# Kernel optimization log

Hardware: AMD Instinct MI355X
Metric: run time of the kernel (lower is better)

Reference implementation:

```python
import jax, jax.numpy as jnp
import numpy as np

B, T, S, D, H = 8, 512, 512, 512, 8
DH = D // H
EPS = 1e-5


def _ln(x, g, b):
    m = x.mean(-1, keepdims=True)
    v = x.var(-1, keepdims=True)
    return (x - m) / jnp.sqrt(v + EPS) * g + b


def setup_inputs() -> dict:
    key = jax.random.key(0)
    ks = jax.random.split(key, 24)
    w = lambda k, shp: (jax.random.normal(k, shp, jnp.float32) * 0.02)
    causal = jnp.where(jnp.tril(jnp.ones((T, T), bool)), 0.0, -1e9).astype(jnp.float32)
    return {
        "tgt": jax.random.normal(ks[0], (B, T, D), jnp.float32),
        "memory": jax.random.normal(ks[1], (B, S, D), jnp.float32),
        "tgt_mask": causal,
        "gate": jax.random.uniform(ks[2], (T, D), jnp.float32),
        # self-attn params (torch MultiheadAttention packed in_proj layout)
        "sa_in_w": w(ks[3], (3 * D, D)), "sa_in_b": w(ks[4], (3 * D,)),
        "sa_out_w": w(ks[5], (D, D)), "sa_out_b": w(ks[6], (D,)),
        # cross-attn params
        "ca_in_w": w(ks[7], (3 * D, D)), "ca_in_b": w(ks[8], (3 * D,)),
        "ca_out_w": w(ks[9], (D, D)), "ca_out_b": w(ks[10], (D,)),
        # FFN
        "ff1_w": w(ks[11], (4 * D, D)), "ff1_b": w(ks[12], (4 * D,)),
        "ff2_w": w(ks[13], (D, 4 * D)), "ff2_b": w(ks[14], (D,)),
        # layernorms
        "ln1_g": jnp.ones((D,), jnp.float32), "ln1_b": jnp.zeros((D,), jnp.float32),
        "ln2_g": jnp.ones((D,), jnp.float32), "ln2_b": jnp.zeros((D,), jnp.float32),
        "ln3_g": jnp.ones((D,), jnp.float32), "ln3_b": jnp.zeros((D,), jnp.float32),
    }


def reference(tgt, memory, tgt_mask, gate,
              sa_in_w, sa_in_b, sa_out_w, sa_out_b,
              ca_in_w, ca_in_b, ca_out_w, ca_out_b,
              ff1_w, ff1_b, ff2_w, ff2_b,
              ln1_g, ln1_b, ln2_g, ln2_b, ln3_g, ln3_b):
    b, t, d = tgt.shape
    s = memory.shape[1]
    scale = 1.0 / jnp.sqrt(jnp.float32(DH))

    # ---- self attention (standard batched MHA, additive mask) ----
    wq, wk, wv = jnp.split(sa_in_w, 3, axis=0)
    bq, bk, bv = jnp.split(sa_in_b, 3, axis=0)
    q = ((tgt @ wq.T + bq).reshape(b, t, H, DH)) * scale
    k = (tgt @ wk.T + bk).reshape(b, t, H, DH)
    v = (tgt @ wv.T + bv).reshape(b, t, H, DH)
    scores = jnp.einsum('bthd,bshd->bhts', q, k) + tgt_mask  # (B,H,T,T)
    attn = jax.nn.softmax(scores, axis=-1)
    sa = jnp.einsum('bhts,bshd->bthd', attn, v).reshape(b, t, d) @ sa_out_w.T + sa_out_b
    x = _ln(tgt + sa, ln1_g, ln1_b)

    # ---- gated cross attention ----
    # Original: key_{b,t,s} = W_k(gate_t * memory_{b,s}) + b_k materialized as (B*T,S,D).
    # Faithful refactor: distribute W_k, fold (q W_k) with gate into the query side.
    cwq, cwk, cwv = jnp.split(ca_in_w, 3, axis=0)
    cbq, cbk, cbv = jnp.split(ca_in_b, 3, axis=0)
    cq = ((x @ cwq.T + cbq).reshape(b, t, H, DH)) * scale          # (B,T,H,dh)
    wk_h = cwk.reshape(H, DH, d)                                    # (H,dh,D)
    qW = jnp.einsum('bthe,hed->bthd', cq, wk_h)                     # (B,T,H,D)
    cscores = jnp.einsum('bthd,td,bsd->bhts', qW, gate, memory)     # (B,H,T,S)
    bk_h = cbk.reshape(H, DH)
    cscores = cscores + jnp.einsum('bthe,he->bht', cq, bk_h)[..., None]
    cattn = jax.nn.softmax(cscores, axis=-1)
    cv = (memory @ cwv.T + cbv).reshape(b, s, H, DH)
    ca = jnp.einsum('bhts,bshe->bthe', cattn, cv).reshape(b, t, d) @ ca_out_w.T + ca_out_b
    x = _ln(x + ca, ln2_g, ln2_b)

    # ---- FFN ----
    ff = jax.nn.relu(x @ ff1_w.T + ff1_b) @ ff2_w.T + ff2_b
    return _ln(x + ff, ln3_g, ln3_b)
```

## Files before the change

kernel.cpp:

```cpp
#include <hip/hip_runtime.h>
#include <hip/hip_bf16.h>

#define BB 8
#define TT 512
#define SS 512
#define DD 512
#define HH 8

typedef __attribute__((ext_vector_type(8))) short bf16x8;
typedef __attribute__((ext_vector_type(4))) float f32x4;
typedef unsigned short u16;

__device__ __forceinline__ u16 f2b(float f) {
    __hip_bfloat16 h = __float2bfloat16(f);
    return *reinterpret_cast<u16*>(&h);
}
__device__ __forceinline__ float b2f(u16 v) {
    unsigned int u = ((unsigned int)v) << 16;
    return __builtin_bit_cast(float, u);
}
__device__ __forceinline__ void g2lds16(const void* g, void* l) {
    __builtin_amdgcn_global_load_lds(
        (const __attribute__((address_space(1))) void*)g,
        (__attribute__((address_space(3))) void*)l, 16, 0, 0);
}
template <int N> __device__ __forceinline__ void waitvm();
template <> __device__ __forceinline__ void waitvm<0>()  { asm volatile("s_waitcnt vmcnt(0)" ::: "memory"); }
template <> __device__ __forceinline__ void waitvm<4>()  { asm volatile("s_waitcnt vmcnt(4)" ::: "memory"); }
template <> __device__ __forceinline__ void waitvm<6>()  { asm volatile("s_waitcnt vmcnt(6)" ::: "memory"); }
template <> __device__ __forceinline__ void waitvm<8>()  { asm volatile("s_waitcnt vmcnt(8)" ::: "memory"); }
template <> __device__ __forceinline__ void waitvm<18>() { asm volatile("s_waitcnt vmcnt(18)" ::: "memory"); }
__device__ __forceinline__ void barrier_raw() {
    asm volatile("" ::: "memory");
    __builtin_amdgcn_s_barrier();
    asm volatile("" ::: "memory");
}

struct CastSegs {
    const float* s[9];
    u16* d[9];
    int cum[10];
};
__global__ __launch_bounds__(256) void cast_multi(CastSegs sg) {
    const int total = sg.cum[9];
    for (int i = blockIdx.x * 256 + threadIdx.x; i < total; i += gridDim.x * 256) {
        int k = 0;
#pragma unroll
        for (int j = 1; j < 9; ++j) k += (i >= sg.cum[j]);
        const int loc = i - sg.cum[k];
        float4 v = ((const float4*)sg.s[k])[loc];
        ushort4 u;
        u.x = f2b(v.x); u.y = f2b(v.y); u.z = f2b(v.z); u.w = f2b(v.w);
        ((ushort4*)sg.d[k])[loc] = u;
    }
}

__global__ __launch_bounds__(256) void wkt_kernel(const float* __restrict__ w,
                                                  u16* __restrict__ o) {
    const int idx = blockIdx.x * 256 + threadIdx.x;
    const int h = idx >> 15, d = (idx >> 6) & 511, e = idx & 63;
    o[idx] = f2b(w[(size_t)(512 + h * 64 + e) * 512 + d]);
}

template <int TM, int TN, bool RELU, bool GATE>
__global__ __launch_bounds__(256) void gemm_bf16(
    const u16* __restrict__ A, int lda, long az,
    const u16* __restrict__ Bw, int ldb, long bz,
    const float* __restrict__ bias, const float* __restrict__ biasB,
    const float* __restrict__ gate,
    u16* __restrict__ C, int ldo, long cz,
    int K, float alpha, float alphaB) {
    __shared__ __align__(16) u16 As[2][TM * 64];
    __shared__ __align__(16) u16 Bs[2][TN * 64];
    const int tid = threadIdx.x;
    const int wave = tid >> 6, lane = tid & 63;
    const int lm = lane & 15, lg = lane >> 4;
    const int wm = wave >> 1, wn = wave & 1;
    const int m0 = blockIdx.y * TM, n0 = blockIdx.x * TN;
    A += (size_t)blockIdx.z * az;
    Bw += (size_t)blockIdx.z * bz;
    C += (size_t)blockIdx.z * cz;
    constexpr int MI = TM / 32;
    constexpr int FN = TN / 32;
    constexpr int LPS = MI + FN;

    f32x4 acc[MI][FN];
#pragma unroll
    for (int mi = 0; mi < MI; ++mi)
#pragma unroll
        for (int ni = 0; ni < FN; ++ni) acc[mi][ni] = (f32x4){0.f, 0.f, 0.f, 0.f};

    const int srow = lane >> 3;
    const int sbyte = ((lane & 7) << 4) ^ (srow << 4);
    const int xk = (lm & 7) << 4;

    auto stage = [&](int buf, int kt) {
#pragma unroll
        for (int j = 0; j < MI; ++j) {
            const int r = wave * (TM / 4) + j * 8;
            g2lds16((const char*)(A + (size_t)(m0 + r + srow) * lda + kt) + sbyte,
                    (char*)As[buf] + (size_t)r * 128);
        }
#pragma unroll
        for (int j = 0; j < FN; ++j) {
            const int r = wave * (TN / 4) + j * 8;
            g2lds16((const char*)(Bw + (size_t)(n0 + r + srow) * ldb + kt) + sbyte,
                    (char*)Bs[buf] + (size_t)r * 128);
        }
    };

    stage(0, 0);
    const int NK = K >> 6;
    for (int t = 0; t < NK; ++t) {
        const int cur = t & 1;
        if (t + 1 < NK) { stage(cur ^ 1, (t + 1) << 6); waitvm<LPS>(); }
        else            { waitvm<0>(); }
        barrier_raw();
#pragma unroll
        for (int kh = 0; kh < 2; ++kh) {
            const int cb = kh * 64 + lg * 16;
            bf16x8 af[MI], bfr[FN];
#pragma unroll
            for (int mi = 0; mi < MI; ++mi) {
                const int row = wm * (TM / 2) + mi * 16 + lm;
                af[mi] = *(const bf16x8*)((const char*)As[cur] + row * 128 + (cb ^ xk));
            }
#pragma unroll
            for (int ni = 0; ni < FN; ++ni) {
                const int row = wn * (TN / 2) + ni * 16 + lm;
                bfr[ni] = *(const bf16x8*)((const char*)Bs[cur] + row * 128 + (cb ^ xk));
            }
#pragma unroll
            for (int mi = 0; mi < MI; ++mi)
#pragma unroll
                for (int ni = 0; ni < FN; ++ni)
                    acc[mi][ni] = __builtin_amdgcn_mfma_f32_16x16x32_bf16(
                        af[mi], bfr[ni], acc[mi][ni], 0, 0, 0);
        }
        barrier_raw();
    }

    const float* bp = blockIdx.z ? biasB : bias;
    const float al = blockIdx.z ? alphaB : alpha;
#pragma unroll
    for (int mi = 0; mi < MI; ++mi)
#pragma unroll
        for (int ni = 0; ni < FN; ++ni)
#pragma unroll
            for (int r = 0; r < 4; ++r) {
                const int m = m0 + wm * (TM / 2) + mi * 16 + lg * 4 + r;
                const int n = n0 + wn * (TN / 2) + ni * 16 + lm;
                float v = acc[mi][ni][r];
                if constexpr (GATE) v *= gate[(size_t)(m & 511) * 512 + n];
                else                v = (v + bp[n]) * al;
                if constexpr (RELU) v = fmaxf(v, 0.f);
                C[(size_t)m * ldo + n] = f2b(v);
            }
}

__global__ __launch_bounds__(256) void flash_self(const u16* __restrict__ QKV,
                                                  u16* __restrict__ out) {
    const int t0 = blockIdx.x * 64, h = blockIdx.y, b = blockIdx.z;
    const int tid = threadIdx.x, wave = tid >> 6, lane = tid & 63;
    const int lm = lane & 15, lg = lane >> 4;
    __shared__ __align__(16) u16 Ks[32 * 64];
    __shared__ __align__(16) u16 Vt[64][40];
    __shared__ __align__(16) u16 P[4][16][40];

    const int tw = t0 + wave * 16;
    const size_t qrow = (size_t)(b * TT + tw + lm) * 1536 + h * 64;
    bf16x8 qf[2];
    qf[0] = *(const bf16x8*)(QKV + qrow + lg * 8);
    qf[1] = *(const bf16x8*)(QKV + qrow + 32 + lg * 8);

    float m_run[4], l_run[4];
    f32x4 oacc[4];
#pragma unroll
    for (int r = 0; r < 4; ++r) { m_run[r] = -3e38f; l_run[r] = 0.f; }
#pragma unroll
    for (int nt = 0; nt < 4; ++nt) oacc[nt] = (f32x4){0.f, 0.f, 0.f, 0.f};

    const int srow = lane >> 3, sbyte = ((lane & 7) << 4) ^ (srow << 4);
    const int xk = (lm & 7) << 4;
    const int smax = t0 + 64;
    for (int s0 = 0; s0 < smax; s0 += 32) {
        if (s0) __syncthreads();
        g2lds16((const char*)(QKV + (size_t)(b * TT + s0 + wave * 8 + srow) * 1536 +
                              512 + h * 64) + sbyte,
                (char*)Ks + wave * 1024);
        {
            const int s = tid & 31, d0 = (tid >> 5) * 8;
            bf16x8 vv = *(const bf16x8*)(QKV + (size_t)(b * TT + s0 + s) * 1536 +
                                         1024 + h * 64 + d0);
#pragma unroll
            for (int j = 0; j < 8; ++j) Vt[d0 + j][s] = (u16)vv[j];
        }
        __syncthreads();
        if (s0 <= tw + 15) {
            f32x4 sc0 = (f32x4){0.f, 0.f, 0.f, 0.f};
            f32x4 sc1 = (f32x4){0.f, 0.f, 0.f, 0.f};
#pragma unroll
            for (int f = 0; f < 2; ++f) {
                const int cb = f * 64 + lg * 16;
                bf16x8 k0 = *(const bf16x8*)((const char*)Ks + lm * 128 + (cb ^ xk));
                bf16x8 k1 = *(const bf16x8*)((const char*)Ks + (16 + lm) * 128 + (cb ^ xk));
                sc0 = __builtin_amdgcn_mfma_f32_16x16x32_bf16(qf[f], k0, sc0, 0, 0, 0);
                sc1 = __builtin_amdgcn_mfma_f32_16x16x32_bf16(qf[f], k1, sc1, 0, 0, 0);
            }
            float sv0[4], sv1[4], tm[4];
#pragma unroll
            for (int r = 0; r < 4; ++r) {
                const int t = tw + lg * 4 + r;
                sv0[r] = sc0[r] * 0.125f + ((s0 + lm) <= t ? 0.f : -1e9f);
                sv1[r] = sc1[r] * 0.125f + ((s0 + 16 + lm) <= t ? 0.f : -1e9f);
                tm[r] = fmaxf(sv0[r], sv1[r]);
            }
#pragma unroll
            for (int off = 1; off < 16; off <<= 1)
#pragma unroll
                for (int r = 0; r < 4; ++r) tm[r] = fmaxf(tm[r], __shfl_xor(tm[r], off));
            float fac[4], rs[4];
#pragma unroll
            for (int r = 0; r < 4; ++r) {
                const float mn = fmaxf(m_run[r], tm[r]);
                fac[r] = __expf(m_run[r] - mn);
                m_run[r] = mn;
                const float p0 = __expf(sv0[r] - mn);
                const float p1 = __expf(sv1[r] - mn);
                P[wave][lg * 4 + r][lm] = f2b(p0);
                P[wave][lg * 4 + r][16 + lm] = f2b(p1);
                rs[r] = p0 + p1;
            }
#pragma unroll
            for (int off = 1; off < 16; off <<= 1)
#pragma unroll
                for (int r = 0; r < 4; ++r) rs[r] += __shfl_xor(rs[r], off);
#pragma unroll
            for (int r = 0; r < 4; ++r) l_run[r] = l_run[r] * fac[r] + rs[r];
#pragma unroll
            for (int nt = 0; nt < 4; ++nt)
#pragma unroll
                for (int r = 0; r < 4; ++r) oacc[nt][r] *= fac[r];
            const bf16x8 pf = *(const bf16x8*)&P[wave][lm][lg * 8];
#pragma unroll
            for (int nt = 0; nt < 4; ++nt) {
                const bf16x8 vf = *(const bf16x8*)&Vt[nt * 16 + lm][lg * 8];
                oacc[nt] = __builtin_amdgcn_mfma_f32_16x16x32_bf16(pf, vf, oacc[nt], 0, 0, 0);
            }
        }
    }
#pragma unroll
    for (int nt = 0; nt < 4; ++nt)
#pragma unroll
        for (int r = 0; r < 4; ++r)
            out[(size_t)(b * TT + tw + lg * 4 + r) * DD + h * 64 + nt * 16 + lm] =
                f2b(oacc[nt][r] / l_run[r]);
}

__global__ __launch_bounds__(128, 2) void flash_cross(
    const u16* __restrict__ QW, const u16* __restrict__ Kmem,
    const u16* __restrict__ CV, u16* __restrict__ out) {
    const int t0 = blockIdx.x * 64, h = blockIdx.y, b = blockIdx.z;
    const int tid = threadIdx.x, wave = tid >> 6, lane = tid & 63;
    const int lm = lane & 15, lg = lane >> 4;
    __shared__ __align__(16) u16 Ks[2][32 * 512];
    __shared__ __align__(16) u16 Vt[2][64][40];
    __shared__ __align__(16) u16 P[2][32][40];

    const int tq = t0 + wave * 32;
    const size_t qrowA = (size_t)(b * TT + tq + lm) * 4096 + h * 512;
    const size_t qrowB = qrowA + (size_t)16 * 4096;
    bf16x8 qfA[16], qfB[16];
#pragma unroll
    for (int f = 0; f < 16; ++f) {
        qfA[f] = *(const bf16x8*)(QW + qrowA + f * 32 + lg * 8);
        qfB[f] = *(const bf16x8*)(QW + qrowB + f * 32 + lg * 8);
    }

    float mA[4], lA[4], mB[4], lB[4];
    f32x4 oA[4], oB[4];
#pragma unroll
    for (int r = 0; r < 4; ++r) { mA[r] = -3e38f; lA[r] = 0.f; mB[r] = -3e38f; lB[r] = 0.f; }
#pragma unroll
    for (int nt = 0; nt < 4; ++nt) { oA[nt] = (f32x4){0.f,0.f,0.f,0.f}; oB[nt] = (f32x4){0.f,0.f,0.f,0.f}; }

    const int xk = (lm & 7) << 4;
    const int sV = tid & 31, dV = (tid >> 5) * 16;

    auto stageK = [&](int buf, int s0) {
#pragma unroll
        for (int j = 0; j < 16; ++j) {
            const int row = wave * 16 + j;
            g2lds16((const char*)(Kmem + ((size_t)b * SS + s0 + row) * 512) +
                        ((lane * 16) ^ ((j & 7) << 4)),
                    (char*)Ks[buf] + row * 1024);
        }
    };
    auto vload0 = [&](int s0) -> bf16x8 {
        return *(const bf16x8*)(CV + ((size_t)b * SS + s0 + sV) * 512 + h * 64 + dV);
    };
    auto vload1 = [&](int s0) -> bf16x8 {
        return *(const bf16x8*)(CV + ((size_t)b * SS + s0 + sV) * 512 + h * 64 + dV + 8);
    };

    stageK(0, 0);
    bf16x8 vr0 = vload0(0), vr1 = vload1(0), vn0, vn1;
    for (int c = 0; c < 16; ++c) {
        const int cur = c & 1;
        if (c + 1 < 16) {
            stageK(cur ^ 1, (c + 1) * 32);
            vn0 = vload0((c + 1) * 32);
            vn1 = vload1((c + 1) * 32);
            waitvm<18>();
        } else {
            waitvm<0>();
        }
#pragma unroll
        for (int j = 0; j < 8; ++j) {
            Vt[cur][dV + j][sV] = (u16)vr0[j];
            Vt[cur][dV + 8 + j][sV] = (u16)vr1[j];
        }
        asm volatile("s_waitcnt lgkmcnt(0)" ::: "memory");
        barrier_raw();
        f32x4 sA0 = (f32x4){0.f,0.f,0.f,0.f}, sA1 = (f32x4){0.f,0.f,0.f,0.f};
        f32x4 sB0 = (f32x4){0.f,0.f,0.f,0.f}, sB1 = (f32x4){0.f,0.f,0.f,0.f};
#pragma unroll
        for (int f = 0; f < 16; ++f) {
            const int cb = f * 64 + lg * 16;
            bf16x8 k0 = *(const bf16x8*)((const char*)Ks[cur] + lm * 1024 + (cb ^ xk));
            bf16x8 k1 = *(const bf16x8*)((const char*)Ks[cur] + (16 + lm) * 1024 + (cb ^ xk));
            sA0 = __builtin_amdgcn_mfma_f32_16x16x32_bf16(qfA[f], k0, sA0, 0, 0, 0);
            sA1 = __builtin_amdgcn_mfma_f32_16x16x32_bf16(qfA[f], k1, sA1, 0, 0, 0);
            sB0 = __builtin_amdgcn_mfma_f32_16x16x32_bf16(qfB[f], k0, sB0, 0, 0, 0);
            sB1 = __builtin_amdgcn_mfma_f32_16x16x32_bf16(qfB[f], k1, sB1, 0, 0, 0);
        }
        float tmA[4], tmB[4];
#pragma unroll
        for (int r = 0; r < 4; ++r) {
            tmA[r] = fmaxf(sA0[r], sA1[r]);
            tmB[r] = fmaxf(sB0[r], sB1[r]);
        }
#pragma unroll
        for (int off = 1; off < 16; off <<= 1)
#pragma unroll
            for (int r = 0; r < 4; ++r) {
                tmA[r] = fmaxf(tmA[r], __shfl_xor(tmA[r], off));
                tmB[r] = fmaxf(tmB[r], __shfl_xor(tmB[r], off));
            }
        float facA[4], facB[4], rsA[4], rsB[4];
#pragma unroll
        for (int r = 0; r < 4; ++r) {
            const float mnA = fmaxf(mA[r], tmA[r]);
            facA[r] = __expf(mA[r] - mnA); mA[r] = mnA;
            const float pA0 = __expf(sA0[r] - mnA);
            const float pA1 = __expf(sA1[r] - mnA);
            P[wave][lg * 4 + r][lm] = f2b(pA0);
            P[wave][lg * 4 + r][16 + lm] = f2b(pA1);
            rsA[r] = pA0 + pA1;
            const float mnB = fmaxf(mB[r], tmB[r]);
            facB[r] = __expf(mB[r] - mnB); mB[r] = mnB;
            const float pB0 = __expf(sB0[r] - mnB);
            const float pB1 = __expf(sB1[r] - mnB);
            P[wave][16 + lg * 4 + r][lm] = f2b(pB0);
            P[wave][16 + lg * 4 + r][16 + lm] = f2b(pB1);
            rsB[r] = pB0 + pB1;
        }
#pragma unroll
        for (int off = 1; off < 16; off <<= 1)
#pragma unroll
            for (int r = 0; r < 4; ++r) {
                rsA[r] += __shfl_xor(rsA[r], off);
                rsB[r] += __shfl_xor(rsB[r], off);
            }
#pragma unroll
        for (int r = 0; r < 4; ++r) {
            lA[r] = lA[r] * facA[r] + rsA[r];
            lB[r] = lB[r] * facB[r] + rsB[r];
        }
#pragma unroll
        for (int nt = 0; nt < 4; ++nt)
#pragma unroll
            for (int r = 0; r < 4; ++r) { oA[nt][r] *= facA[r]; oB[nt][r] *= facB[r]; }
        const bf16x8 pfA = *(const bf16x8*)&P[wave][lm][lg * 8];
        const bf16x8 pfB = *(const bf16x8*)&P[wave][16 + lm][lg * 8];
#pragma unroll
        for (int nt = 0; nt < 4; ++nt) {
            const bf16x8 vf = *(const bf16x8*)&Vt[cur][nt * 16 + lm][lg * 8];
            oA[nt] = __builtin_amdgcn_mfma_f32_16x16x32_bf16(pfA, vf, oA[nt], 0, 0, 0);
            oB[nt] = __builtin_amdgcn_mfma_f32_16x16x32_bf16(pfB, vf, oB[nt], 0, 0, 0);
        }
        barrier_raw();
        vr0 = vn0; vr1 = vn1;
    }
#pragma unroll
    for (int nt = 0; nt < 4; ++nt)
#pragma unroll
        for (int r = 0; r < 4; ++r) {
            out[(size_t)(b * TT + tq + lg * 4 + r) * DD + h * 64 + nt * 16 + lm] =
                f2b(oA[nt][r] / lA[r]);
            out[(size_t)(b * TT + tq + 16 + lg * 4 + r) * DD + h * 64 + nt * 16 + lm] =
                f2b(oB[nt][r] / lB[r]);
        }
}

template <bool R1B>
__global__ __launch_bounds__(256) void add_ln(
    const void* __restrict__ R1v, const u16* __restrict__ R2,
    const float* __restrict__ g, const float* __restrict__ bta,
    float* __restrict__ outf, u16* __restrict__ outb) {
    const int row = blockIdx.x, tid = threadIdx.x;
    float x0, x1;
    if constexpr (R1B) {
        ushort2 a = ((const ushort2*)((const u16*)R1v + (size_t)row * DD))[tid];
        x0 = b2f(a.x); x1 = b2f(a.y);
    } else {
        float2 a = ((const float2*)((const float*)R1v + (size_t)row * DD))[tid];
        x0 = a.x; x1 = a.y;
    }
    ushort2 c = ((const ushort2*)(R2 + (size_t)row * DD))[tid];
    x0 += b2f(c.x); x1 += b2f(c.y);

    __shared__ float2 red[256];
    red[tid] = make_float2(x0 + x1, x0 * x0 + x1 * x1);
    __syncthreads();
#pragma unroll
    for (int o = 128; o > 0; o >>= 1) {
        if (tid < o) {
            red[tid].x += red[tid + o].x;
            red[tid].y += red[tid + o].y;
        }
        __syncthreads();
    }
    const float mean = red[0].x * (1.f / 512.f);
    const float var = red[0].y * (1.f / 512.f) - mean * mean;
    const float rstd = rsqrtf(var + 1e-5f);
    const int i = tid * 2;
    const float y0 = (x0 - mean) * rstd * g[i] + bta[i];
    const float y1 = (x1 - mean) * rstd * g[i + 1] + bta[i + 1];
    if (outf) ((float2*)(outf + (size_t)row * DD))[tid] = make_float2(y0, y1);
    if (outb) {
        ushort2 ub; ub.x = f2b(y0); ub.y = f2b(y1);
        ((ushort2*)(outb + (size_t)row * DD))[tid] = ub;
    }
}

extern "C" void kernel_launch(void* const* d_in, const int* in_sizes, int n_in,
                              void* d_out, int out_size, void* d_ws, size_t ws_size,
                              hipStream_t stream) {
    const float* tgt      = (const float*)d_in[0];
    const float* memory   = (const float*)d_in[1];
    const float* gate     = (const float*)d_in[3];
    const float* sa_in_w  = (const float*)d_in[4];
    const float* sa_in_b  = (const float*)d_in[5];
    const float* sa_out_w = (const float*)d_in[6];
    const float* sa_out_b = (const float*)d_in[7];
    const float* ca_in_w  = (const float*)d_in[8];
    const float* ca_in_b  = (const float*)d_in[9];
    const float* ca_out_w = (const float*)d_in[10];
    const float* ca_out_b = (const float*)d_in[11];
    const float* ff1_w    = (const float*)d_in[12];
    const float* ff1_b    = (const float*)d_in[13];
    const float* ff2_w    = (const float*)d_in[14];
    const float* ff2_b    = (const float*)d_in[15];
    const float* ln1_g    = (const float*)d_in[16];
    const float* ln1_b    = (const float*)d_in[17];
    const float* ln2_g    = (const float*)d_in[18];
    const float* ln2_b    = (const float*)d_in[19];
    const float* ln3_g    = (const float*)d_in[20];
    const float* ln3_b    = (const float*)d_in[21];

    u16* ws16     = (u16*)d_ws;
    u16* QKVb     = ws16;
    u16* sa_preb  = ws16 + 6291456;
    u16* PRJb     = ws16 + 8388608;
    u16* X1b      = ws16 + 10485760;
    u16* memb     = ws16 + 12582912;
    u16* CQb      = ws16 + 14680064;
    u16* CVb      = ws16 + 16777216;
    u16* QW       = ws16 + 18874368;
    u16* ca_preb  = ws16 + 35651584;
    u16* PRJ2b    = ws16 + 37748736;
    u16* X2b      = ws16 + 39845888;
    u16* HHb      = ws16 + 41943040;
    u16* F1b      = ws16 + 50331648;
    u16* Wreg     = ws16 + 52428800;
    u16* sa_in_wb = Wreg;
    u16* sa_out_wb= Wreg + 786432;
    u16* ca_wq_b  = Wreg + 1048576;
    u16* ca_wv_b  = Wreg + 1310720;
    u16* WkT      = Wreg + 1572864;
    u16* ca_out_wb= Wreg + 1835008;
    u16* ff1_wb   = Wreg + 2097152;
    u16* ff2_wb   = Wreg + 3145728;
    u16* tgtb     = ws16 + 56623104;
    float* outf   = (float*)d_out;

    const dim3 blk(256);

    CastSegs sg;
    sg.s[0]=tgt; sg.s[1]=memory; sg.s[2]=sa_in_w; sg.s[3]=sa_out_w;
    sg.s[4]=ca_in_w; sg.s[5]=ca_in_w + (size_t)1024*512; sg.s[6]=ca_out_w;
    sg.s[7]=ff1_w; sg.s[8]=ff2_w;
    sg.d[0]=tgtb; sg.d[1]=memb; sg.d[2]=sa_in_wb; sg.d[3]=sa_out_wb;
    sg.d[4]=ca_wq_b; sg.d[5]=ca_wv_b; sg.d[6]=ca_out_wb;
    sg.d[7]=ff1_wb; sg.d[8]=ff2_wb;
    {
        const int n4[9] = {524288,524288,196608,65536,65536,65536,65536,262144,262144};
        int c = 0;
        for (int i = 0; i < 9; ++i) { sg.cum[i] = c; c += n4[i]; }
        sg.cum[9] = c;
    }
    cast_multi<<<2048, blk, 0, stream>>>(sg);
    wkt_kernel<<<1024, blk, 0, stream>>>(ca_in_w, WkT);

    gemm_bf16<128,128,false,false><<<dim3(12,32,1), blk, 0, stream>>>(
        tgtb,512,0, sa_in_wb,512,0, sa_in_b,sa_in_b,nullptr,
        QKVb,1536,0, 512, 1.f,1.f);
    flash_self<<<dim3(8,8,8), blk, 0, stream>>>(QKVb, sa_preb);
    gemm_bf16<64,64,false,false><<<dim3(8,64,1), blk, 0, stream>>>(
        sa_preb,512,0, sa_out_wb,512,0, sa_out_b,sa_out_b,nullptr,
        PRJb,512,0, 512, 1.f,1.f);
    add_ln<false><<<4096, blk, 0, stream>>>(tgt, PRJb, ln1_g, ln1_b, nullptr, X1b);
    gemm_bf16<64,64,false,false><<<dim3(8,64,2), blk, 0, stream>>>(
        X1b,512,2097152, ca_wq_b,512,262144, ca_in_b, ca_in_b+1024, nullptr,
        CQb,512,2097152, 512, 0.125f, 1.f);
    gemm_bf16<64,64,false,true><<<dim3(8,64,8), blk, 0, stream>>>(
        CQb,512,64, WkT,64,32768, nullptr,nullptr,gate,
        QW,4096,512, 64, 1.f,1.f);
    flash_cross<<<dim3(8,8,8), dim3(128), 0, stream>>>(QW, memb, CVb, ca_preb);
    gemm_bf16<64,64,false,false><<<dim3(8,64,1), blk, 0, stream>>>(
        ca_preb,512,0, ca_out_wb,512,0, ca_out_b,ca_out_b,nullptr,
        PRJ2b,512,0, 512, 1.f,1.f);
    add_ln<true><<<4096, blk, 0, stream>>>(X1b, PRJ2b, ln2_g, ln2_b, nullptr, X2b);
    gemm_bf16<128,128,true,false><<<dim3(16,32,1), blk, 0, stream>>>(
        X2b,512,0, ff1_wb,512,0, ff1_b,ff1_b,nullptr,
        HHb,2048,0, 512, 1.f,1.f);
    gemm_bf16<64,64,false,false><<<dim3(8,64,1), blk, 0, stream>>>(
        HHb,2048,0, ff2_wb,2048,0, ff2_b,ff2_b,nullptr,
        F1b,512,0, 2048, 1.f,1.f);
    add_ln<true><<<4096, blk, 0, stream>>>(X2b, F1b, ln3_g, ln3_b, outf, nullptr);

    (void)in_sizes; (void)n_in; (void)out_size; (void)ws_size;
}
```

Baseline: 219.6 us.

## Single-buffer K tile in flash_cross and overlap its load with softmax

Cuts the cross-attention K staging buffer in LDS from double to single buffering, roughly halving per-block shared memory so more blocks can be resident per CU. It also drops the min-blocks launch bound. The prefetch of the next K and V chunk is moved to just after the QK MFMAs and a barrier, so it overlaps with the softmax and PV work instead of the whole previous iteration. The cost is less overlap time before the wait at the end of each iteration, which could expose load latency, plus an extra barrier per chunk.

```diff
diff --git a/kernel.cpp b/kernel.cpp
--- a/kernel.cpp
+++ b/kernel.cpp
@@ -29,7 +29,7 @@
 template <> __device__ __forceinline__ void waitvm<4>()  { asm volatile("s_waitcnt vmcnt(4)" ::: "memory"); }
 template <> __device__ __forceinline__ void waitvm<6>()  { asm volatile("s_waitcnt vmcnt(6)" ::: "memory"); }
 template <> __device__ __forceinline__ void waitvm<8>()  { asm volatile("s_waitcnt vmcnt(8)" ::: "memory"); }
-template <> __device__ __forceinline__ void waitvm<18>() { asm volatile("s_waitcnt vmcnt(18)" ::: "memory"); }
+template <> __device__ __forceinline__ void waitvm<16>() { asm volatile("s_waitcnt vmcnt(16)" ::: "memory"); }
 __device__ __forceinline__ void barrier_raw() {
     asm volatile("" ::: "memory");
     __builtin_amdgcn_s_barrier();
@@ -257,13 +257,13 @@
                 f2b(oacc[nt][r] / l_run[r]);
 }
 
-__global__ __launch_bounds__(128, 2) void flash_cross(
+__global__ __launch_bounds__(128) void flash_cross(
     const u16* __restrict__ QW, const u16* __restrict__ Kmem,
     const u16* __restrict__ CV, u16* __restrict__ out) {
     const int t0 = blockIdx.x * 64, h = blockIdx.y, b = blockIdx.z;
     const int tid = threadIdx.x, wave = tid >> 6, lane = tid & 63;
     const int lm = lane & 15, lg = lane >> 4;
-    __shared__ __align__(16) u16 Ks[2][32 * 512];
+    __shared__ __align__(16) u16 Ks[32 * 512];
     __shared__ __align__(16) u16 Vt[2][64][40];
     __shared__ __align__(16) u16 P[2][32][40];
 
@@ -287,13 +287,13 @@
     const int xk = (lm & 7) << 4;
     const int sV = tid & 31, dV = (tid >> 5) * 16;
 
-    auto stageK = [&](int buf, int s0) {
+    auto stageK = [&](int s0) {
 #pragma unroll
         for (int j = 0; j < 16; ++j) {
             const int row = wave * 16 + j;
             g2lds16((const char*)(Kmem + ((size_t)b * SS + s0 + row) * 512) +
                         ((lane * 16) ^ ((j & 7) << 4)),
-                    (char*)Ks[buf] + row * 1024);
+                    (char*)Ks + row * 1024);
         }
     };
     auto vload0 = [&](int s0) -> bf16x8 {
@@ -303,36 +303,36 @@
         return *(const bf16x8*)(CV + ((size_t)b * SS + s0 + sV) * 512 + h * 64 + dV + 8);
     };
 
-    stageK(0, 0);
-    bf16x8 vr0 = vload0(0), vr1 = vload1(0), vn0, vn1;
+    bf16x8 vr0 = vload0(0), vr1 = vload1(0);
+    stageK(0);
+    waitvm<0>();
+#pragma unroll
+    for (int j = 0; j < 8; ++j) {
+        Vt[0][dV + j][sV] = (u16)vr0[j];
+        Vt[0][dV + 8 + j][sV] = (u16)vr1[j];
+    }
+    asm volatile("s_waitcnt lgkmcnt(0)" ::: "memory");
+    barrier_raw();
+
     for (int c = 0; c < 16; ++c) {
         const int cur = c & 1;
-        if (c + 1 < 16) {
-            stageK(cur ^ 1, (c + 1) * 32);
-            vn0 = vload0((c + 1) * 32);
-            vn1 = vload1((c + 1) * 32);
-            waitvm<18>();
-        } else {
-            waitvm<0>();
-        }
-#pragma unroll
-        for (int j = 0; j < 8; ++j) {
-            Vt[cur][dV + j][sV] = (u16)vr0[j];
-            Vt[cur][dV + 8 + j][sV] = (u16)vr1[j];
-        }
-        asm volatile("s_waitcnt lgkmcnt(0)" ::: "memory");
-        barrier_raw();
         f32x4 sA0 = (f32x4){0.f,0.f,0.f,0.f}, sA1 = (f32x4){0.f,0.f,0.f,0.f};
         f32x4 sB0 = (f32x4){0.f,0.f,0.f,0.f}, sB1 = (f32x4){0.f,0.f,0.f,0.f};
 #pragma unroll
         for (int f = 0; f < 16; ++f) {
             const int cb = f * 64 + lg * 16;
-            bf16x8 k0 = *(const bf16x8*)((const char*)Ks[cur] + lm * 1024 + (cb ^ xk));
-            bf16x8 k1 = *(const bf16x8*)((const char*)Ks[cur] + (16 + lm) * 1024 + (cb ^ xk));
+            bf16x8 k0 = *(const bf16x8*)((const char*)Ks + lm * 1024 + (cb ^ xk));
+            bf16x8 k1 = *(const bf16x8*)((const char*)Ks + (16 + lm) * 1024 + (cb ^ xk));
             sA0 = __builtin_amdgcn_mfma_f32_16x16x32_bf16(qfA[f], k0, sA0, 0, 0, 0);
             sA1 = __builtin_amdgcn_mfma_f32_16x16x32_bf16(qfA[f], k1, sA1, 0, 0, 0);
             sB0 = __builtin_amdgcn_mfma_f32_16x16x32_bf16(qfB[f], k0, sB0, 0, 0, 0);
             sB1 = __builtin_amdgcn_mfma_f32_16x16x32_bf16(qfB[f], k1, sB1, 0, 0, 0);
+        }
+        barrier_raw();
+        if (c < 15) {
+            vr0 = vload0((c + 1) * 32);
+            vr1 = vload1((c + 1) * 32);
+            stageK((c + 1) * 32);
         }
         float tmA[4], tmB[4];
 #pragma unroll
@@ -389,8 +389,17 @@
             oA[nt] = __builtin_amdgcn_mfma_f32_16x16x32_bf16(pfA, vf, oA[nt], 0, 0, 0);
             oB[nt] = __builtin_amdgcn_mfma_f32_16x16x32_bf16(pfB, vf, oB[nt], 0, 0, 0);
         }
-        barrier_raw();
-        vr0 = vn0; vr1 = vn1;
+        if (c < 15) {
+            waitvm<16>();
+#pragma unroll
+            for (int j = 0; j < 8; ++j) {
+                Vt[cur ^ 1][dV + j][sV] = (u16)vr0[j];
+                Vt[cur ^ 1][dV + 8 + j][sV] = (u16)vr1[j];
+            }
+            waitvm<0>();
+            asm volatile("s_waitcnt lgkmcnt(0)" ::: "memory");
+            barrier_raw();
+        }
     }
 #pragma unroll
     for (int nt = 0; nt < 4; ++nt)
```

Measured after the change: 227.1 us. 3.4% more time.

## Split fused cross-attention into scores GEMM plus separate softmax-PV kernel

Applied to the files above, without the earlier changes.

Replaces the fused flash-style cross attention (K-dim 512 per head, low occupancy, 128-thread blocks) with two kernels. A tiled 128x128 GEMM writes full fp32 score matrices to workspace, then a second kernel does a single-pass softmax and the P·V MFMA with V held transposed in LDS. This trades the online-softmax bookkeeping and poor tile reuse for a large round trip of fp32 scores through global memory (64 MB written and read) and one extra launch.

```diff
diff --git a/kernel.cpp b/kernel.cpp
--- a/kernel.cpp
+++ b/kernel.cpp
@@ -29,7 +29,6 @@
 template <> __device__ __forceinline__ void waitvm<4>()  { asm volatile("s_waitcnt vmcnt(4)" ::: "memory"); }
 template <> __device__ __forceinline__ void waitvm<6>()  { asm volatile("s_waitcnt vmcnt(6)" ::: "memory"); }
 template <> __device__ __forceinline__ void waitvm<8>()  { asm volatile("s_waitcnt vmcnt(8)" ::: "memory"); }
-template <> __device__ __forceinline__ void waitvm<18>() { asm volatile("s_waitcnt vmcnt(18)" ::: "memory"); }
 __device__ __forceinline__ void barrier_raw() {
     asm volatile("" ::: "memory");
     __builtin_amdgcn_s_barrier();
@@ -158,6 +157,166 @@
             }
 }
 
+__global__ __launch_bounds__(256) void gemm_scores(
+    const u16* __restrict__ QWp, const u16* __restrict__ membp,
+    float* __restrict__ SC) {
+    __shared__ __align__(16) u16 As[2][128 * 64];
+    __shared__ __align__(16) u16 Bs[2][128 * 64];
+    const int tid = threadIdx.x;
+    const int wave = tid >> 6, lane = tid & 63;
+    const int lm = lane & 15, lg = lane >> 4;
+    const int wm = wave >> 1, wn = wave & 1;
+    const int m0 = blockIdx.y * 128, n0 = blockIdx.x * 128;
+    const int z = blockIdx.z, b = z >> 3, h = z & 7;
+    const u16* A  = QWp + (size_t)b * TT * 4096 + h * 512;
+    const u16* Bw = membp + (size_t)b * SS * 512;
+    float* C = SC + ((size_t)z << 18);
+
+    f32x4 acc[4][4];
+#pragma unroll
+    for (int mi = 0; mi < 4; ++mi)
+#pragma unroll
+        for (int ni = 0; ni < 4; ++ni) acc[mi][ni] = (f32x4){0.f, 0.f, 0.f, 0.f};
+
+    const int srow = lane >> 3;
+    const int sbyte = ((lane & 7) << 4) ^ (srow << 4);
+    const int xk = (lm & 7) << 4;
+
+    auto stage = [&](int buf, int kt) {
+#pragma unroll
+        for (int j = 0; j < 4; ++j) {
+            const int r = wave * 32 + j * 8;
+            g2lds16((const char*)(A + (size_t)(m0 + r + srow) * 4096 + kt) + sbyte,
+                    (char*)As[buf] + (size_t)r * 128);
+            g2lds16((const char*)(Bw + (size_t)(n0 + r + srow) * 512 + kt) + sbyte,
+                    (char*)Bs[buf] + (size_t)r * 128);
+        }
+    };
+
+    stage(0, 0);
+    for (int t = 0; t < 8; ++t) {
+        const int cur = t & 1;
+        if (t + 1 < 8) { stage(cur ^ 1, (t + 1) << 6); waitvm<8>(); }
+        else           { waitvm<0>(); }
+        barrier_raw();
+#pragma unroll
+        for (int kh = 0; kh < 2; ++kh) {
+            const int cb = kh * 64 + lg * 16;
+            bf16x8 af[4], bfr[4];
+#pragma unroll
+            for (int mi = 0; mi < 4; ++mi) {
+                const int row = wm * 64 + mi * 16 + lm;
+                af[mi] = *(const bf16x8*)((const char*)As[cur] + row * 128 + (cb ^ xk));
+            }
+#pragma unroll
+            for (int ni = 0; ni < 4; ++ni) {
+                const int row = wn * 64 + ni * 16 + lm;
+                bfr[ni] = *(const bf16x8*)((const char*)Bs[cur] + row * 128 + (cb ^ xk));
+            }
+#pragma unroll
+            for (int mi = 0; mi < 4; ++mi)
+#pragma unroll
+                for (int ni = 0; ni < 4; ++ni)
+                    acc[mi][ni] = __builtin_amdgcn_mfma_f32_16x16x32_bf16(
+                        af[mi], bfr[ni], acc[mi][ni], 0, 0, 0);
+        }
+        barrier_raw();
+    }
+#pragma unroll
+    for (int mi = 0; mi < 4; ++mi)
+#pragma unroll
+        for (int ni = 0; ni < 4; ++ni)
+#pragma unroll
+            for (int r = 0; r < 4; ++r) {
+                const int m = m0 + wm * 64 + mi * 16 + lg * 4 + r;
+                const int n = n0 + wn * 64 + ni * 16 + lm;
+                C[(size_t)m * 512 + n] = acc[mi][ni][r];
+            }
+}
+
+__global__ __launch_bounds__(256) void softmax_pv(
+    const float* __restrict__ SC, const u16* __restrict__ CV,
+    u16* __restrict__ out) {
+    const int t0 = blockIdx.x * 64, h = blockIdx.y, b = blockIdx.z;
+    const int tid = threadIdx.x, wave = tid >> 6, lane = tid & 63;
+    const int lm = lane & 15, lg = lane >> 4;
+    __shared__ __align__(16) u16 Vt[64 * 512];
+
+    {
+        const int sp = tid * 2;
+#pragma unroll
+        for (int c = 0; c < 8; ++c) {
+            bf16x8 v0 = *(const bf16x8*)(CV + ((size_t)b * SS + sp) * 512 + h * 64 + c * 8);
+            bf16x8 v1 = *(const bf16x8*)(CV + ((size_t)b * SS + sp + 1) * 512 + h * 64 + c * 8);
+#pragma unroll
+            for (int j = 0; j < 8; ++j) {
+                const int d = c * 8 + j;
+                const unsigned int pk = (unsigned int)(u16)v0[j] |
+                                        ((unsigned int)(u16)v1[j] << 16);
+                *(unsigned int*)((char*)Vt + ((d << 10) + ((sp * 2) ^ ((d & 7) << 4)))) = pk;
+            }
+        }
+    }
+
+    const int tw = t0 + wave * 16;
+    const float* srow = SC + ((size_t)(b * 8 + h) << 18) + (size_t)(tw + lm) * 512 + lg * 8;
+    float4 sa[16][2];
+#pragma unroll
+    for (int k = 0; k < 16; ++k) {
+        sa[k][0] = *(const float4*)(srow + k * 32);
+        sa[k][1] = *(const float4*)(srow + k * 32 + 4);
+    }
+    float mx = -3e38f;
+#pragma unroll
+    for (int k = 0; k < 16; ++k) {
+        mx = fmaxf(mx, fmaxf(fmaxf(sa[k][0].x, sa[k][0].y), fmaxf(sa[k][0].z, sa[k][0].w)));
+        mx = fmaxf(mx, fmaxf(fmaxf(sa[k][1].x, sa[k][1].y), fmaxf(sa[k][1].z, sa[k][1].w)));
+    }
+    mx = fmaxf(mx, __shfl_xor(mx, 16));
+    mx = fmaxf(mx, __shfl_xor(mx, 32));
+    float sum = 0.f;
+    bf16x8 pb[16];
+#pragma unroll
+    for (int k = 0; k < 16; ++k) {
+        float p0 = __expf(sa[k][0].x - mx), p1 = __expf(sa[k][0].y - mx);
+        float p2 = __expf(sa[k][0].z - mx), p3 = __expf(sa[k][0].w - mx);
+        float p4 = __expf(sa[k][1].x - mx), p5 = __expf(sa[k][1].y - mx);
+        float p6 = __expf(sa[k][1].z - mx), p7 = __expf(sa[k][1].w - mx);
+        sum += (p0 + p1 + p2 + p3) + (p4 + p5 + p6 + p7);
+        pb[k][0] = (short)f2b(p0); pb[k][1] = (short)f2b(p1);
+        pb[k][2] = (short)f2b(p2); pb[k][3] = (short)f2b(p3);
+        pb[k][4] = (short)f2b(p4); pb[k][5] = (short)f2b(p5);
+        pb[k][6] = (short)f2b(p6); pb[k][7] = (short)f2b(p7);
+    }
+    sum += __shfl_xor(sum, 16);
+    sum += __shfl_xor(sum, 32);
+
+    __syncthreads();
+
+    f32x4 o[4];
+#pragma unroll
+    for (int nt = 0; nt < 4; ++nt) o[nt] = (f32x4){0.f, 0.f, 0.f, 0.f};
+#pragma unroll
+    for (int k = 0; k < 16; ++k) {
+#pragma unroll
+        for (int nt = 0; nt < 4; ++nt) {
+            const int d = nt * 16 + lm;
+            const bf16x8 vf = *(const bf16x8*)((const char*)Vt +
+                ((d << 10) + ((k * 64 + lg * 16) ^ ((d & 7) << 4))));
+            o[nt] = __builtin_amdgcn_mfma_f32_16x16x32_bf16(pb[k], vf, o[nt], 0, 0, 0);
+        }
+    }
+#pragma unroll
+    for (int r = 0; r < 4; ++r) {
+        const float rs = __shfl(sum, lg * 4 + r);
+        const float inv = 1.f / rs;
+#pragma unroll
+        for (int nt = 0; nt < 4; ++nt)
+            out[(size_t)(b * TT + tw + lg * 4 + r) * DD + h * 64 + nt * 16 + lm] =
+                f2b(o[nt][r] * inv);
+    }
+}
+
 __global__ __launch_bounds__(256) void flash_self(const u16* __restrict__ QKV,
                                                   u16* __restrict__ out) {
     const int t0 = blockIdx.x * 64, h = blockIdx.y, b = blockIdx.z;
@@ -255,152 +414,6 @@
         for (int r = 0; r < 4; ++r)
             out[(size_t)(b * TT + tw + lg * 4 + r) * DD + h * 64 + nt * 16 + lm] =
                 f2b(oacc[nt][r] / l_run[r]);
-}
-
-__global__ __launch_bounds__(128, 2) void flash_cross(
-    const u16* __restrict__ QW, const u16* __restrict__ Kmem,
-    const u16* __restrict__ CV, u16* __restrict__ out) {
-    const int t0 = blockIdx.x * 64, h = blockIdx.y, b = blockIdx.z;
-    const int tid = threadIdx.x, wave = tid >> 6, lane = tid & 63;
-    const int lm = lane & 15, lg = lane >> 4;
-    __shared__ __align__(16) u16 Ks[2][32 * 512];
-    __shared__ __align__(16) u16 Vt[2][64][40];
-    __shared__ __align__(16) u16 P[2][32][40];
-
-    const int tq = t0 + wave * 32;
-    const size_t qrowA = (size_t)(b * TT + tq + lm) * 4096 + h * 512;
-    const size_t qrowB = qrowA + (size_t)16 * 4096;
-    bf16x8 qfA[16], qfB[16];
-#pragma unroll
-    for (int f = 0; f < 16; ++f) {
-        qfA[f] = *(const bf16x8*)(QW + qrowA + f * 32 + lg * 8);
-        qfB[f] = *(const bf16x8*)(QW + qrowB + f * 32 + lg * 8);
-    }
-
-    float mA[4], lA[4], mB[4], lB[4];
-    f32x4 oA[4], oB[4];
-#pragma unroll
-    for (int r = 0; r < 4; ++r) { mA[r] = -3e38f; lA[r] = 0.f; mB[r] = -3e38f; lB[r] = 0.f; }
-#pragma unroll
-    for (int nt = 0; nt < 4; ++nt) { oA[nt] = (f32x4){0.f,0.f,0.f,0.f}; oB[nt] = (f32x4){0.f,0.f,0.f,0.f}; }
-
-    const int xk = (lm & 7) << 4;
-    const int sV = tid & 31, dV = (tid >> 5) * 16;
-
-    auto stageK = [&](int buf, int s0) {
-#pragma unroll
-        for (int j = 0; j < 16; ++j) {
-            const int row = wave * 16 + j;
-            g2lds16((const char*)(Kmem + ((size_t)b * SS + s0 + row) * 512) +
-                        ((lane * 16) ^ ((j & 7) << 4)),
-                    (char*)Ks[buf] + row * 1024);
-        }
-    };
-    auto vload0 = [&](int s0) -> bf16x8 {
-        return *(const bf16x8*)(CV + ((size_t)b * SS + s0 + sV) * 512 + h * 64 + dV);
-    };
-    auto vload1 = [&](int s0) -> bf16x8 {
-        return *(const bf16x8*)(CV + ((size_t)b * SS + s0 + sV) * 512 + h * 64 + dV + 8);
-    };
-
-    stageK(0, 0);
-    bf16x8 vr0 = vload0(0), vr1 = vload1(0), vn0, vn1;
-    for (int c = 0; c < 16; ++c) {
-        const int cur = c & 1;
-        if (c + 1 < 16) {
-            stageK(cur ^ 1, (c + 1) * 32);
-            vn0 = vload0((c + 1) * 32);
-            vn1 = vload1((c + 1) * 32);
-            waitvm<18>();
-        } else {
-            waitvm<0>();
-        }
-#pragma unroll
-        for (int j = 0; j < 8; ++j) {
-            Vt[cur][dV + j][sV] = (u16)vr0[j];
-            Vt[cur][dV + 8 + j][sV] = (u16)vr1[j];
-        }
-        asm volatile("s_waitcnt lgkmcnt(0)" ::: "memory");
-        barrier_raw();
-        f32x4 sA0 = (f32x4){0.f,0.f,0.f,0.f}, sA1 = (f32x4){0.f,0.f,0.f,0.f};
-        f32x4 sB0 = (f32x4){0.f,0.f,0.f,0.f}, sB1 = (f32x4){0.f,0.f,0.f,0.f};
-#pragma unroll
-        for (int f = 0; f < 16; ++f) {
-            const int cb = f * 64 + lg * 16;
-            bf16x8 k0 = *(const bf16x8*)((const char*)Ks[cur] + lm * 1024 + (cb ^ xk));
-            bf16x8 k1 = *(const bf16x8*)((const char*)Ks[cur] + (16 + lm) * 1024 + (cb ^ xk));
-            sA0 = __builtin_amdgcn_mfma_f32_16x16x32_bf16(qfA[f], k0, sA0, 0, 0, 0);
-            sA1 = __builtin_amdgcn_mfma_f32_16x16x32_bf16(qfA[f], k1, sA1, 0, 0, 0);
-            sB0 = __builtin_amdgcn_mfma_f32_16x16x32_bf16(qfB[f], k0, sB0, 0, 0, 0);
-            sB1 = __builtin_amdgcn_mfma_f32_16x16x32_bf16(qfB[f], k1, sB1, 0, 0, 0);
-        }
-        float tmA[4], tmB[4];
-#pragma unroll
-        for (int r = 0; r < 4; ++r) {
-            tmA[r] = fmaxf(sA0[r], sA1[r]);
-            tmB[r] = fmaxf(sB0[r], sB1[r]);
-        }
-#pragma unroll
-        for (int off = 1; off < 16; off <<= 1)
-#pragma unroll
-            for (int r = 0; r < 4; ++r) {
-                tmA[r] = fmaxf(tmA[r], __shfl_xor(tmA[r], off));
-                tmB[r] = fmaxf(tmB[r], __shfl_xor(tmB[r], off));
-            }
-        float facA[4], facB[4], rsA[4], rsB[4];
-#pragma unroll
-        for (int r = 0; r < 4; ++r) {
-            const float mnA = fmaxf(mA[r], tmA[r]);
-            facA[r] = __expf(mA[r] - mnA); mA[r] = mnA;
-            const float pA0 = __expf(sA0[r] - mnA);
-            const float pA1 = __expf(sA1[r] - mnA);
-            P[wave][lg * 4 + r][lm] = f2b(pA0);
-            P[wave][lg * 4 + r][16 + lm] = f2b(pA1);
-            rsA[r] = pA0 + pA1;
-            const float mnB = fmaxf(mB[r], tmB[r]);
-            facB[r] = __expf(mB[r] - mnB); mB[r] = mnB;
-            const float pB0 = __expf(sB0[r] - mnB);
-            const float pB1 = __expf(sB1[r] - mnB);
-            P[wave][16 + lg * 4 + r][lm] = f2b(pB0);
-            P[wave][16 + lg * 4 + r][16 + lm] = f2b(pB1);
-            rsB[r] = pB0 + pB1;
-        }
-#pragma unroll
-        for (int off = 1; off < 16; off <<= 1)
-#pragma unroll
-            for (int r = 0; r < 4; ++r) {
-                rsA[r] += __shfl_xor(rsA[r], off);
-                rsB[r] += __shfl_xor(rsB[r], off);
-            }
-#pragma unroll
-        for (int r = 0; r < 4; ++r) {
-            lA[r] = lA[r] * facA[r] + rsA[r];
-            lB[r] = lB[r] * facB[r] + rsB[r];
-        }
-#pragma unroll
-        for (int nt = 0; nt < 4; ++nt)
-#pragma unroll
-            for (int r = 0; r < 4; ++r) { oA[nt][r] *= facA[r]; oB[nt][r] *= facB[r]; }
-        const bf16x8 pfA = *(const bf16x8*)&P[wave][lm][lg * 8];
-        const bf16x8 pfB = *(const bf16x8*)&P[wave][16 + lm][lg * 8];
-#pragma unroll
-        for (int nt = 0; nt < 4; ++nt) {
-            const bf16x8 vf = *(const bf16x8*)&Vt[cur][nt * 16 + lm][lg * 8];
-            oA[nt] = __builtin_amdgcn_mfma_f32_16x16x32_bf16(pfA, vf, oA[nt], 0, 0, 0);
-            oB[nt] = __builtin_amdgcn_mfma_f32_16x16x32_bf16(pfB, vf, oB[nt], 0, 0, 0);
-        }
-        barrier_raw();
-        vr0 = vn0; vr1 = vn1;
-    }
-#pragma unroll
-    for (int nt = 0; nt < 4; ++nt)
-#pragma unroll
-        for (int r = 0; r < 4; ++r) {
-            out[(size_t)(b * TT + tq + lg * 4 + r) * DD + h * 64 + nt * 16 + lm] =
-                f2b(oA[nt][r] / lA[r]);
-            out[(size_t)(b * TT + tq + 16 + lg * 4 + r) * DD + h * 64 + nt * 16 + lm] =
-                f2b(oB[nt][r] / lB[r]);
-        }
 }
 
 template <bool R1B>
@@ -493,6 +506,7 @@
     u16* ff1_wb   = Wreg + 2097152;
     u16* ff2_wb   = Wreg + 3145728;
     u16* tgtb     = ws16 + 56623104;
+    float* SC     = (float*)(ws16 + 58720256);
     float* outf   = (float*)d_out;
 
     const dim3 blk(256);
@@ -527,7 +541,8 @@
     gemm_bf16<64,64,false,true><<<dim3(8,64,8), blk, 0, stream>>>(
         CQb,512,64, WkT,64,32768, nullptr,nullptr,gate,
         QW,4096,512, 64, 1.f,1.f);
-    flash_cross<<<dim3(8,8,8), dim3(128), 0, stream>>>(QW, memb, CVb, ca_preb);
+    gemm_scores<<<dim3(4,4,64), blk, 0, stream>>>(QW, memb, SC);
+    softmax_pv<<<dim3(8,8,8), blk, 0, stream>>>(SC, CVb, ca_preb);
     gemm_bf16<64,64,false,false><<<dim3(8,64,1), blk, 0, stream>>>(
         ca_preb,512,0, ca_out_wb,512,0, ca_out_b,ca_out_b,nullptr,
         PRJ2b,512,0, 512, 1.f,1.f);
```

Result: faster. 214.9 us (-2.2%).
